# Kernel tuning notes

Measured on AMD Instinct MI355X. Metric: run time of the kernel, lower is better.

The kernel has to match this reference:

```python
import jax, jax.numpy as jnp
import numpy as np

BATCH = 65536
SEQ_LEN = 1024  # matrix_size**2
DEGREE = 7


def chebvander(t, deg):
    """Chebyshev Vandermonde matrix: T_0..T_deg evaluated at t. Returns [..., deg+1]."""
    cols = [jnp.ones_like(t), t]
    for _ in range(2, deg + 1):
        cols.append(2.0 * t * cols[-1] - cols[-2])
    return jnp.stack(cols[: deg + 1], axis=-1)


def setup_inputs() -> dict:
    key = jax.random.key(0)
    x = jax.random.normal(key, (BATCH, SEQ_LEN), dtype=jnp.float32)
    # strictly increasing time grid over the natural Chebyshev domain [-1, 1]
    time_grid = jnp.linspace(-1.0, 1.0, SEQ_LEN, dtype=jnp.float32)
    return {"x": x, "time_grid": time_grid}


def reference(x, time_grid):
    B, L = x.shape
    M = int(np.sqrt(L))          # matrix_size (32)
    # values[b, i, j] = x[b, i + j*M]  -> reshape to (M_j, M_i) then transpose
    values = x.reshape(B, M, M).transpose(0, 2, 1)          # [B, i, j]
    times = time_grid.reshape(M, M).T                        # [i, j]
    # Chebyshev least-squares fit per row i (same times for every batch element):
    V = chebvander(times, DEGREE)                            # [i, j, D]
    G = jnp.einsum('ijd,ije->ide', V, V)                     # [M, D, D] Gram matrices
    rhs = jnp.einsum('ijd,bij->bid', V, values)              # [B, M, D]
    # normal-equation solve == lstsq solution for well-conditioned Vandermonde
    coeffs = jnp.linalg.solve(G[None], rhs[..., None])[..., 0]  # [B, M, D]
    return coeffs
```

## Files before the change

kernel.cpp:

```cpp
#include <hip/hip_runtime.h>

#define MM 32
#define DD 8
#define LL 1024
#define NBATCH 65536
#define NBLK 2048
#define RPB (NBATCH / NBLK)
#define NPASS (RPB / 2)

__device__ float g_Wt[MM * DD * MM];

__global__ void precompute_w_kernel(const float* __restrict__ tg) {
    const int i = blockIdx.x;
    const int t = threadIdx.x;

    __shared__ float  V[MM][DD];
    __shared__ double A[DD][2 * DD];

    if (t < MM) {
        float tt = tg[t * MM + i];
        float c0 = 1.0f, c1 = tt;
        V[t][0] = c0;
        V[t][1] = c1;
        for (int e = 2; e < DD; ++e) {
            float c2 = 2.0f * tt * c1 - c0;
            V[t][e] = c2;
            c0 = c1; c1 = c2;
        }
    }
    __syncthreads();

    {
        int d = t >> 3, e = t & 7;
        double s = 0.0;
        for (int j = 0; j < MM; ++j) s += (double)V[j][d] * (double)V[j][e];
        A[d][e] = s;
        A[d][DD + e] = (d == e) ? 1.0 : 0.0;
    }
    __syncthreads();

    if (t == 0) {
        for (int p = 0; p < DD; ++p) {
            double inv = 1.0 / A[p][p];
            for (int c = p; c < 2 * DD; ++c) A[p][c] *= inv;
            for (int r2 = 0; r2 < DD; ++r2) {
                if (r2 == p) continue;
                double f = A[r2][p];
                for (int c = p; c < 2 * DD; ++c) A[r2][c] -= f * A[p][c];
            }
        }
    }
    __syncthreads();

    for (int k = t; k < DD * MM; k += 64) {
        int d = k >> 5;
        int j = k & 31;
        double s = 0.0;
        for (int e = 0; e < DD; ++e) s += A[d][DD + e] * (double)V[j][e];
        g_Wt[(i * DD + d) * MM + j] = (float)s;
    }
}

__global__ __launch_bounds__(256, 4) void poly_apply_kernel(
        const float* __restrict__ x,
        float* __restrict__ out) {
    __shared__ __align__(16) float xT[2][2][1152];

    const int t   = threadIdx.x;
    const int rs  = t >> 7;
    const int tt  = t & 127;
    const int si  = tt & 31;
    const int sq  = tt >> 5;
    const int ci  = tt >> 2;
    const int dp  = t & 3;

    float w0[32], w1[32];
    {
        const float4* wp = (const float4*)g_Wt + (ci * DD + 2 * dp) * 8;
#pragma unroll
        for (int q = 0; q < 8; ++q) {
            float4 a = wp[q];
            w0[4 * q + 0] = a.x; w0[4 * q + 1] = a.y;
            w0[4 * q + 2] = a.z; w0[4 * q + 3] = a.w;
            float4 b = wp[q + 8];
            w1[4 * q + 0] = b.x; w1[4 * q + 1] = b.y;
            w1[4 * q + 2] = b.z; w1[4 * q + 3] = b.w;
        }
    }
#pragma unroll
    for (int j = 0; j < 32; ++j) {
        asm volatile("" : "+v"(w0[j]));
        asm volatile("" : "+v"(w1[j]));
    }

    const int r0 = blockIdx.x * RPB;
    const float* xbase = x + (size_t)(r0 + rs) * LL + si + 256 * sq;
    const int wboff = si * 36 + 8 * sq;

    float v[8];

#pragma unroll
    for (int c = 0; c < 8; ++c) v[c] = xbase[32 * c];
    {
        float* wb = &xT[0][rs][wboff];
#pragma unroll
        for (int k = 0; k < 4; ++k) {
            float2 p2; p2.x = v[2 * k]; p2.y = v[2 * k + 1];
            *(float2*)&wb[2 * k] = p2;
        }
    }
#pragma unroll
    for (int c = 0; c < 8; ++c) v[c] = xbase[2 * LL + 32 * c];
    __syncthreads();

    for (int p = 0; p < NPASS; ++p) {
        if (p + 1 < NPASS) {
            float* wb = &xT[(p + 1) & 1][rs][wboff];
#pragma unroll
            for (int k = 0; k < 4; ++k) {
                float2 p2; p2.x = v[2 * k]; p2.y = v[2 * k + 1];
                *(float2*)&wb[2 * k] = p2;
            }
        }
        if (p + 2 < NPASS) {
#pragma unroll
            for (int c = 0; c < 8; ++c)
                v[c] = xbase[(size_t)(p + 2) * 2 * LL + 32 * c];
        }

        {
            const float* xb = &xT[p & 1][rs][ci * 36];
            float a0 = 0.f, a1 = 0.f;
#pragma unroll
            for (int m = 0; m < 8; ++m) {
                float4 xq = *(const float4*)&xb[4 * m];
                a0 = fmaf(w0[4 * m + 0], xq.x, a0);
                a1 = fmaf(w1[4 * m + 0], xq.x, a1);
                a0 = fmaf(w0[4 * m + 1], xq.y, a0);
                a1 = fmaf(w1[4 * m + 1], xq.y, a1);
                a0 = fmaf(w0[4 * m + 2], xq.z, a0);
                a1 = fmaf(w1[4 * m + 2], xq.z, a1);
                a0 = fmaf(w0[4 * m + 3], xq.w, a0);
                a1 = fmaf(w1[4 * m + 3], xq.w, a1);
            }
            float2 o; o.x = a0; o.y = a1;
            *(float2*)&out[(size_t)(r0 + 2 * p + rs) * 256 + ci * 8 + 2 * dp] = o;
        }

        __syncthreads();
    }
}

extern "C" void kernel_launch(void* const* d_in, const int* in_sizes, int n_in,
                              void* d_out, int out_size, void* d_ws, size_t ws_size,
                              hipStream_t stream) {
    const float* x  = (const float*)d_in[0];
    const float* tg = (const float*)d_in[1];
    float* out = (float*)d_out;
    (void)d_ws; (void)ws_size;

    precompute_w_kernel<<<32, 64, 0, stream>>>(tg);
    poly_apply_kernel<<<NBLK, 256, 0, stream>>>(x, out);
}
```

Before: 397.1 us.

## Give each wavefront a private LDS buffer and drop block-wide barriers

Reorganizes the apply kernel so each 64-lane wavefront owns its own double-buffered LDS tile. Each wave covers half of the 32 row groups for a 32-row batch slab, and the per-pass __syncthreads is removed because only that wave touches its buffer. The grid is halved to 1024 blocks, each handling 64 batch rows, and the asm register-pinning hints are dropped. The aim is to remove barrier stalls in a latency-bound streaming loop. In exchange, global loads now move in 16-float contiguous segments instead of 32, and correctness relies on wave-local LDS ordering without explicit barriers.

```diff
diff --git a/kernel.cpp b/kernel.cpp
--- a/kernel.cpp
+++ b/kernel.cpp
@@ -4,9 +4,8 @@
 #define DD 8
 #define LL 1024
 #define NBATCH 65536
-#define NBLK 2048
-#define RPB (NBATCH / NBLK)
-#define NPASS (RPB / 2)
+#define NBLK 1024
+#define NPASS 32
 
 __device__ float g_Wt[MM * DD * MM];
 
@@ -64,19 +63,20 @@
 __global__ __launch_bounds__(256, 4) void poly_apply_kernel(
         const float* __restrict__ x,
         float* __restrict__ out) {
-    __shared__ __align__(16) float xT[2][2][1152];
+    __shared__ __align__(16) float xT[4][2][580];
 
-    const int t   = threadIdx.x;
-    const int rs  = t >> 7;
-    const int tt  = t & 127;
-    const int si  = tt & 31;
-    const int sq  = tt >> 5;
-    const int ci  = tt >> 2;
-    const int dp  = t & 3;
+    const int t  = threadIdx.x;
+    const int w  = t >> 6;
+    const int l  = t & 63;
+    const int ih = w & 1;
+    const int iw = l >> 2;
+    const int dp = l & 3;
+
+    const int rbase = blockIdx.x * 64 + (w >> 1) * 32;
 
     float w0[32], w1[32];
     {
-        const float4* wp = (const float4*)g_Wt + (ci * DD + 2 * dp) * 8;
+        const float4* wp = (const float4*)g_Wt + ((ih * 16 + iw) * DD + 2 * dp) * 8;
 #pragma unroll
         for (int q = 0; q < 8; ++q) {
             float4 a = wp[q];
@@ -87,49 +87,33 @@
             w1[4 * q + 2] = b.z; w1[4 * q + 3] = b.w;
         }
     }
-#pragma unroll
-    for (int j = 0; j < 32; ++j) {
-        asm volatile("" : "+v"(w0[j]));
-        asm volatile("" : "+v"(w1[j]));
-    }
 
-    const int r0 = blockIdx.x * RPB;
-    const float* xbase = x + (size_t)(r0 + rs) * LL + si + 256 * sq;
-    const int wboff = si * 36 + 8 * sq;
+    const int soff  = ih * 16 + (l & 15) + 32 * (l >> 4);
+    const float* xp = x + (size_t)rbase * LL + soff;
+    const int swoff = (l & 15) * 36 + (l >> 4);
 
     float v[8];
 
 #pragma unroll
-    for (int c = 0; c < 8; ++c) v[c] = xbase[32 * c];
-    {
-        float* wb = &xT[0][rs][wboff];
+    for (int c = 0; c < 8; ++c) v[c] = xp[128 * c];
 #pragma unroll
-        for (int k = 0; k < 4; ++k) {
-            float2 p2; p2.x = v[2 * k]; p2.y = v[2 * k + 1];
-            *(float2*)&wb[2 * k] = p2;
-        }
-    }
+    for (int c = 0; c < 8; ++c) xT[w][0][swoff + 4 * c] = v[c];
 #pragma unroll
-    for (int c = 0; c < 8; ++c) v[c] = xbase[2 * LL + 32 * c];
-    __syncthreads();
+    for (int c = 0; c < 8; ++c) v[c] = xp[LL + 128 * c];
 
+#pragma unroll 2
     for (int p = 0; p < NPASS; ++p) {
         if (p + 1 < NPASS) {
-            float* wb = &xT[(p + 1) & 1][rs][wboff];
 #pragma unroll
-            for (int k = 0; k < 4; ++k) {
-                float2 p2; p2.x = v[2 * k]; p2.y = v[2 * k + 1];
-                *(float2*)&wb[2 * k] = p2;
-            }
+            for (int c = 0; c < 8; ++c) xT[w][(p + 1) & 1][swoff + 4 * c] = v[c];
         }
         if (p + 2 < NPASS) {
 #pragma unroll
-            for (int c = 0; c < 8; ++c)
-                v[c] = xbase[(size_t)(p + 2) * 2 * LL + 32 * c];
+            for (int c = 0; c < 8; ++c) v[c] = xp[(size_t)(p + 2) * LL + 128 * c];
         }
 
         {
-            const float* xb = &xT[p & 1][rs][ci * 36];
+            const float* xb = &xT[w][p & 1][iw * 36];
             float a0 = 0.f, a1 = 0.f;
 #pragma unroll
             for (int m = 0; m < 8; ++m) {
@@ -144,10 +128,8 @@
                 a1 = fmaf(w1[4 * m + 3], xq.w, a1);
             }
             float2 o; o.x = a0; o.y = a1;
-            *(float2*)&out[(size_t)(r0 + 2 * p + rs) * 256 + ci * 8 + 2 * dp] = o;
+            *(float2*)&out[(size_t)(rbase + p) * 256 + (ih * 16 + iw) * 8 + 2 * dp] = o;
         }
-
-        __syncthreads();
     }
 }
 
```

After: 399.9 us. About the same (+0.7%).
